# Performance work log

Hardware: AMD Instinct MI355X
Metric: run time of the kernel (lower is better)

The kernel has to match this reference:

```python
import jax, jax.numpy as jnp
import numpy as np

B, H, S, DK, DV = 4, 16, 8192, 128, 128

def setup_inputs() -> dict:
    key = jax.random.key(0)
    k1, k2, k3, k4 = jax.random.split(key, 4)
    return {
        "K": jax.random.normal(k1, (B, H, S, DK), dtype=jnp.float32),
        "V": jax.random.normal(k2, (B, H, S, DV), dtype=jnp.float32),
        "M": jax.random.normal(k3, (B, H, DK, DV), dtype=jnp.float32),
        "z": jax.random.uniform(k4, (B, H, DK), dtype=jnp.float32),
    }

def reference(K, V, M, z):
    # phi = ELU(K) + 1  (positive feature map)
    phi_K = jax.nn.elu(K) + 1.0                                   # (B,H,S,dk)
    V_existing = jnp.einsum('bhsk,bhkv->bhsv', phi_K, M)          # (B,H,S,dv)
    delta_M = jnp.einsum('bhsk,bhsv->bhkv', phi_K, V - V_existing)
    new_M = M + delta_M                                           # (B,H,dk,dv)
    new_z = z + phi_K.sum(axis=-2)                                # (B,H,dk)
    return new_M, new_z
```

## Files before the change

kernel.cpp:

```cpp
#include <hip/hip_runtime.h>

#define BH 64
#define SEQ 8192
#define DK 128
#define DV 128
#define CS 64
#define LR 72

typedef _Float16 f16;
typedef _Float16 f16x4 __attribute__((ext_vector_type(4)));
typedef _Float16 f16x8 __attribute__((ext_vector_type(8)));
typedef float f32x4 __attribute__((ext_vector_type(4)));

template <int NC, bool PARTIAL>
__global__ __launch_bounds__(512, 4) void delta_phase1(
    const float* __restrict__ Kg, const float* __restrict__ Vg,
    float* __restrict__ dstP,
    float* __restrict__ dstG,
    float* __restrict__ newZ)
{
  __shared__ f16 phi_lds[DK * LR];
  __shared__ f16 v_lds[DV * LR];

  constexpr int SC  = SEQ / NC;
  constexpr int NST = SC / CS;

  const int chunk = blockIdx.x;
  const int bh    = blockIdx.y;
  const int tid   = threadIdx.x;
  const int wave  = tid >> 6;
  const int lane  = tid & 63;
  const int l31   = lane & 31;
  const int lhi   = lane >> 5;
  const int f15_  = lane & 15;
  const int quad  = lane >> 4;

  const float* Kh = Kg + ((size_t)bh * SEQ + (size_t)chunk * SC) * DK;
  const float* Vh = Vg + ((size_t)bh * SEQ + (size_t)chunk * SC) * DV;
  const int srow = wave * 8 + lhi * 4;

  f32x4 acc[8][2];
#pragma unroll
  for (int r = 0; r < 8; ++r)
#pragma unroll
    for (int c = 0; c < 2; ++c)
      acc[r][c] = (f32x4){0.f, 0.f, 0.f, 0.f};

  float zacc[4] = {0.f, 0.f, 0.f, 0.f};

  float kr[16], vr[16];
#define LOAD_STAGE(ST)                                              \
  {                                                                 \
    const float* Ks_ = Kh + (size_t)(ST) * CS * DK;                 \
    const float* Vs_ = Vh + (size_t)(ST) * CS * DV;                 \
    _Pragma("unroll")                                               \
    for (int fj = 0; fj < 4; ++fj) {                                \
      const int feat_ = fj * 32 + l31;                              \
      const float* kp_ = Ks_ + (size_t)srow * DK + feat_;           \
      const float* vp_ = Vs_ + (size_t)srow * DV + feat_;           \
      _Pragma("unroll")                                             \
      for (int j = 0; j < 4; ++j) {                                 \
        kr[fj * 4 + j] = kp_[(size_t)j * DK];                       \
        vr[fj * 4 + j] = vp_[(size_t)j * DV];                       \
      }                                                             \
    }                                                               \
  }

  LOAD_STAGE(0);

  for (int st = 0; st < NST; ++st) {
#pragma unroll
    for (int fj = 0; fj < 4; ++fj) {
      const int feat = fj * 32 + l31;
      const float a0 = kr[fj * 4 + 0];
      const float a1 = kr[fj * 4 + 1];
      const float a2 = kr[fj * 4 + 2];
      const float a3 = kr[fj * 4 + 3];
      const float p0 = a0 > 0.f ? a0 + 1.f : __expf(a0);
      const float p1 = a1 > 0.f ? a1 + 1.f : __expf(a1);
      const float p2 = a2 > 0.f ? a2 + 1.f : __expf(a2);
      const float p3 = a3 > 0.f ? a3 + 1.f : __expf(a3);
      zacc[fj] += (p0 + p1) + (p2 + p3);
      *(f16x4*)&phi_lds[feat * LR + srow] =
          (f16x4){(f16)p0, (f16)p1, (f16)p2, (f16)p3};
      *(f16x4*)&v_lds[feat * LR + srow] =
          (f16x4){(f16)vr[fj * 4 + 0], (f16)vr[fj * 4 + 1],
                  (f16)vr[fj * 4 + 2], (f16)vr[fj * 4 + 3]};
    }
    __syncthreads();

    if (st + 1 < NST) LOAD_STAGE(st + 1);

    const f16* bsrc  = (wave < 4) ? v_lds : phi_lds;
    const int  cbase = (wave < 4) ? wave * 32 : wave * 32 - 128;
    __builtin_amdgcn_s_setprio(1);
#pragma unroll
    for (int ss = 0; ss < 2; ++ss) {
      const int sb = ss * 32 + quad * 8;
      f16x8 bfr[2];
#pragma unroll
      for (int c = 0; c < 2; ++c)
        bfr[c] = *(const f16x8*)&bsrc[(cbase + c * 16 + f15_) * LR + sb];
#pragma unroll
      for (int r = 0; r < 8; ++r) {
        const f16x8 afr = *(const f16x8*)&phi_lds[(r * 16 + f15_) * LR + sb];
        acc[r][0] = __builtin_amdgcn_mfma_f32_16x16x32_f16(afr, bfr[0], acc[r][0], 0, 0, 0);
        acc[r][1] = __builtin_amdgcn_mfma_f32_16x16x32_f16(afr, bfr[1], acc[r][1], 0, 0, 0);
      }
    }
    __builtin_amdgcn_s_setprio(0);
    __syncthreads();
  }
#undef LOAD_STAGE

  if (PARTIAL) {
    const size_t pb = (size_t)(bh * NC + chunk) * (128 * 256);
#pragma unroll
    for (int r = 0; r < 8; ++r)
#pragma unroll
      for (int c = 0; c < 2; ++c) {
        const int col = wave * 32 + c * 16 + f15_;
#pragma unroll
        for (int q = 0; q < 4; ++q) {
          const int row = r * 16 + quad * 4 + q;
          dstP[pb + (size_t)row * 256 + col] = acc[r][c][q];
        }
      }
  } else {
    const size_t mb = (size_t)bh * DK * DV;
#pragma unroll
    for (int r = 0; r < 8; ++r)
#pragma unroll
      for (int c = 0; c < 2; ++c) {
        const int col = wave * 32 + c * 16 + f15_;
#pragma unroll
        for (int q = 0; q < 4; ++q) {
          const int row = r * 16 + quad * 4 + q;
          const float v = acc[r][c][q];
          if (col < DV)
            atomicAdd(&dstP[mb + (size_t)row * DV + col], v);
          else
            atomicAdd(&dstG[mb + (size_t)row * DK + (col - DV)], v);
        }
      }
  }
#pragma unroll
  for (int fj = 0; fj < 4; ++fj) {
    float v = zacc[fj];
    v += __shfl_xor(v, 32, 64);
    if (lhi == 0) atomicAdd(&newZ[bh * DK + fj * 32 + l31], v);
  }
}

__global__ __launch_bounds__(256) void delta_reduce(
    const float* __restrict__ Pp, const float* __restrict__ Mg,
    float* __restrict__ newM, float* __restrict__ Gred, int NC)
{
  const int ct  = blockIdx.x;
  const int bh  = blockIdx.y;
  const int tid = threadIdx.x;
  const int col = ct * 32 + (tid & 31);
  const int r0  = tid >> 5;

  float acc[16];
#pragma unroll
  for (int i = 0; i < 16; ++i) acc[i] = 0.f;

  const float* base = Pp + (size_t)(bh * NC) * 32768;
  for (int ch = 0; ch < NC; ++ch) {
    const float* p = base + (size_t)ch * 32768;
#pragma unroll
    for (int i = 0; i < 16; ++i)
      acc[i] += p[(size_t)(r0 + 8 * i) * 256 + col];
  }
  if (col < 128) {
#pragma unroll
    for (int i = 0; i < 16; ++i) {
      const int row = r0 + 8 * i;
      newM[(size_t)bh * 16384 + (size_t)row * 128 + col] =
          Mg[(size_t)bh * 16384 + (size_t)row * 128 + col] + acc[i];
    }
  } else {
#pragma unroll
    for (int i = 0; i < 16; ++i) {
      const int row = r0 + 8 * i;
      Gred[(size_t)bh * 16384 + (size_t)row * 128 + (col - 128)] = acc[i];
    }
  }
}

__global__ __launch_bounds__(256) void delta_gm(
    const float* __restrict__ Mg, const float* __restrict__ G, float* __restrict__ newM)
{
  __shared__ float Gs[64 * 129];
  __shared__ float Ms[DK * 32];
  const int sub = blockIdx.x;
  const int bh  = blockIdx.y;
  const int kh  = sub >> 2;
  const int vt  = sub & 3;
  const int tid = threadIdx.x;
  const size_t mb = (size_t)bh * DK * DV;

  for (int i = tid; i < 64 * DK; i += 256)
    Gs[(i >> 7) * 129 + (i & 127)] = G[mb + (size_t)(kh * 64 + (i >> 7)) * DK + (i & 127)];
  for (int i = tid; i < DK * 32; i += 256)
    Ms[i] = Mg[mb + (size_t)(i >> 5) * DV + vt * 32 + (i & 31)];
  __syncthreads();

  const int kl = tid >> 2;
  const int vs = (tid & 3) * 8;
  float a[8];
#pragma unroll
  for (int j = 0; j < 8; ++j) a[j] = 0.f;
  for (int kk = 0; kk < DK; ++kk) {
    const float g = Gs[kl * 129 + kk];
#pragma unroll
    for (int j = 0; j < 8; ++j) a[j] += g * Ms[kk * 32 + vs + j];
  }
  float* dst = &newM[mb + (size_t)(kh * 64 + kl) * DV + vt * 32 + vs];
#pragma unroll
  for (int j = 0; j < 8; ++j) dst[j] -= a[j];
}

extern "C" void kernel_launch(void* const* d_in, const int* in_sizes, int n_in,
                              void* d_out, int out_size, void* d_ws, size_t ws_size,
                              hipStream_t stream) {
  const float* Kg = (const float*)d_in[0];
  const float* Vg = (const float*)d_in[1];
  const float* Mg = (const float*)d_in[2];
  const float* zg = (const float*)d_in[3];
  float* out  = (float*)d_out;
  float* newM = out;
  float* newZ = out + (size_t)BH * DK * DV;

  const size_t gredF = (size_t)BH * DK * DK;
  const size_t need8 = ((size_t)BH * 8 * 32768 + gredF) * sizeof(float);

  hipMemcpyAsync(newZ, zg, sizeof(float) * (size_t)BH * DK,
                 hipMemcpyDeviceToDevice, stream);

  if (ws_size >= need8) {
    float* Pp   = (float*)d_ws;
    float* Gred = Pp + (size_t)BH * 8 * 32768;
    delta_phase1<8, true><<<dim3(8, BH), 512, 0, stream>>>(Kg, Vg, Pp, nullptr, newZ);
    delta_reduce<<<dim3(8, BH), 256, 0, stream>>>(Pp, Mg, newM, Gred, 8);
    delta_gm<<<dim3(8, BH), 256, 0, stream>>>(Mg, Gred, newM);
  } else {
    float* Gws = (float*)d_ws;
    hipMemcpyAsync(newM, Mg, sizeof(float) * (size_t)BH * DK * DV,
                   hipMemcpyDeviceToDevice, stream);
    hipMemsetAsync(Gws, 0, sizeof(float) * gredF, stream);
    delta_phase1<8, false><<<dim3(8, BH), 512, 0, stream>>>(Kg, Vg, newM, Gws, newZ);
    delta_gm<<<dim3(8, BH), 256, 0, stream>>>(Mg, Gws, newM);
  }
}
```

Baseline: 565.6 us.

## Use float4 loads, smaller stages with register double-buffering, and XOR-swizzled LDS

Phase 1 now processes 32-row stages instead of 64. Each thread issues vectorized float4 global loads of four consecutive features, rather than strided scalar loads. Two register sets alternate so the next stage loads while the current one converts and runs MFMA, and barriers are raw s_barrier calls with lgkmcnt waits. LDS indices are XOR-swizzled to reduce bank conflicts on the transposed f16x2 stores and f16x8 reads. The cost is more barriers per row processed and less MFMA work per stage.

```diff
diff --git a/kernel.cpp b/kernel.cpp
--- a/kernel.cpp
+++ b/kernel.cpp
@@ -4,11 +4,11 @@
 #define SEQ 8192
 #define DK 128
 #define DV 128
-#define CS 64
+#define CS 32
 #define LR 72
 
 typedef _Float16 f16;
-typedef _Float16 f16x4 __attribute__((ext_vector_type(4)));
+typedef _Float16 f16x2 __attribute__((ext_vector_type(2)));
 typedef _Float16 f16x8 __attribute__((ext_vector_type(8)));
 typedef float f32x4 __attribute__((ext_vector_type(4)));
 
@@ -24,20 +24,24 @@
 
   constexpr int SC  = SEQ / NC;
   constexpr int NST = SC / CS;
+  static_assert(NST % 2 == 0, "double-buffer needs even stage count");
 
   const int chunk = blockIdx.x;
   const int bh    = blockIdx.y;
   const int tid   = threadIdx.x;
   const int wave  = tid >> 6;
   const int lane  = tid & 63;
-  const int l31   = lane & 31;
-  const int lhi   = lane >> 5;
+  const int c32   = lane & 31;
+  const int chi   = lane >> 5;
   const int f15_  = lane & 15;
   const int quad  = lane >> 4;
 
   const float* Kh = Kg + ((size_t)bh * SEQ + (size_t)chunk * SC) * DK;
   const float* Vh = Vg + ((size_t)bh * SEQ + (size_t)chunk * SC) * DV;
-  const int srow = wave * 8 + lhi * 4;
+
+  const int srow0    = wave * 4 + chi * 2;
+  const int featbase = c32 * 4;
+  const int swx      = ((c32 >> 1) & 7) << 3;
 
   f32x4 acc[8][2];
 #pragma unroll
@@ -48,70 +52,80 @@
 
   float zacc[4] = {0.f, 0.f, 0.f, 0.f};
 
-  float kr[16], vr[16];
-#define LOAD_STAGE(ST)                                              \
-  {                                                                 \
-    const float* Ks_ = Kh + (size_t)(ST) * CS * DK;                 \
-    const float* Vs_ = Vh + (size_t)(ST) * CS * DV;                 \
-    _Pragma("unroll")                                               \
-    for (int fj = 0; fj < 4; ++fj) {                                \
-      const int feat_ = fj * 32 + l31;                              \
-      const float* kp_ = Ks_ + (size_t)srow * DK + feat_;           \
-      const float* vp_ = Vs_ + (size_t)srow * DV + feat_;           \
-      _Pragma("unroll")                                             \
-      for (int j = 0; j < 4; ++j) {                                 \
-        kr[fj * 4 + j] = kp_[(size_t)j * DK];                       \
-        vr[fj * 4 + j] = vp_[(size_t)j * DV];                       \
-      }                                                             \
-    }                                                               \
-  }
-
-  LOAD_STAGE(0);
-
-  for (int st = 0; st < NST; ++st) {
-#pragma unroll
-    for (int fj = 0; fj < 4; ++fj) {
-      const int feat = fj * 32 + l31;
-      const float a0 = kr[fj * 4 + 0];
-      const float a1 = kr[fj * 4 + 1];
-      const float a2 = kr[fj * 4 + 2];
-      const float a3 = kr[fj * 4 + 3];
-      const float p0 = a0 > 0.f ? a0 + 1.f : __expf(a0);
-      const float p1 = a1 > 0.f ? a1 + 1.f : __expf(a1);
-      const float p2 = a2 > 0.f ? a2 + 1.f : __expf(a2);
-      const float p3 = a3 > 0.f ? a3 + 1.f : __expf(a3);
-      zacc[fj] += (p0 + p1) + (p2 + p3);
-      *(f16x4*)&phi_lds[feat * LR + srow] =
-          (f16x4){(f16)p0, (f16)p1, (f16)p2, (f16)p3};
-      *(f16x4*)&v_lds[feat * LR + srow] =
-          (f16x4){(f16)vr[fj * 4 + 0], (f16)vr[fj * 4 + 1],
-                  (f16)vr[fj * 4 + 2], (f16)vr[fj * 4 + 3]};
-    }
-    __syncthreads();
-
-    if (st + 1 < NST) LOAD_STAGE(st + 1);
-
-    const f16* bsrc  = (wave < 4) ? v_lds : phi_lds;
-    const int  cbase = (wave < 4) ? wave * 32 : wave * 32 - 128;
-    __builtin_amdgcn_s_setprio(1);
-#pragma unroll
-    for (int ss = 0; ss < 2; ++ss) {
-      const int sb = ss * 32 + quad * 8;
-      f16x8 bfr[2];
-#pragma unroll
-      for (int c = 0; c < 2; ++c)
-        bfr[c] = *(const f16x8*)&bsrc[(cbase + c * 16 + f15_) * LR + sb];
-#pragma unroll
-      for (int r = 0; r < 8; ++r) {
-        const f16x8 afr = *(const f16x8*)&phi_lds[(r * 16 + f15_) * LR + sb];
-        acc[r][0] = __builtin_amdgcn_mfma_f32_16x16x32_f16(afr, bfr[0], acc[r][0], 0, 0, 0);
-        acc[r][1] = __builtin_amdgcn_mfma_f32_16x16x32_f16(afr, bfr[1], acc[r][1], 0, 0, 0);
-      }
-    }
-    __builtin_amdgcn_s_setprio(0);
-    __syncthreads();
+  f32x4 ka0, ka1, va0, va1;
+  f32x4 kb0, kb1, vb0, vb1;
+
+#define LOAD_STAGE(ST, K0, K1, V0, V1)                                   \
+  {                                                                      \
+    const float* kp_ = Kh + ((size_t)(ST) * CS + srow0) * DK + featbase; \
+    const float* vp_ = Vh + ((size_t)(ST) * CS + srow0) * DV + featbase; \
+    K0 = *(const f32x4*)kp_;                                             \
+    K1 = *(const f32x4*)(kp_ + DK);                                      \
+    V0 = *(const f32x4*)vp_;                                             \
+    V1 = *(const f32x4*)(vp_ + DV);                                      \
+  }
+
+#define CONVERT_STORE(K0, K1, V0, V1)                                    \
+  {                                                                      \
+    _Pragma("unroll")                                                    \
+    for (int ff = 0; ff < 4; ++ff) {                                     \
+      const int feat = featbase + ff;                                    \
+      const float a0 = K0[ff], a1 = K1[ff];                              \
+      const float p0 = a0 > 0.f ? a0 + 1.f : __expf(a0);                 \
+      const float p1 = a1 > 0.f ? a1 + 1.f : __expf(a1);                 \
+      zacc[ff] += p0 + p1;                                               \
+      const int idx = (feat * LR + srow0) ^ swx;                         \
+      *(f16x2*)&phi_lds[idx] = (f16x2){(f16)p0, (f16)p1};                \
+      *(f16x2*)&v_lds[idx]   = (f16x2){(f16)V0[ff], (f16)V1[ff]};        \
+    }                                                                    \
+  }
+
+#define BAR()                                                            \
+  {                                                                      \
+    asm volatile("s_waitcnt lgkmcnt(0)" ::: "memory");                   \
+    __builtin_amdgcn_s_barrier();                                        \
+  }
+
+#define MFMA_PHASE()                                                     \
+  {                                                                      \
+    const f16* bsrc  = (wave < 4) ? v_lds : phi_lds;                     \
+    const int  cbase = (wave < 4) ? wave * 32 : wave * 32 - 128;         \
+    const int  sb    = quad * 8;                                         \
+    __builtin_amdgcn_s_setprio(1);                                       \
+    f16x8 bfr[2];                                                        \
+    _Pragma("unroll")                                                    \
+    for (int c = 0; c < 2; ++c) {                                        \
+      const int fB = cbase + c * 16 + f15_;                              \
+      bfr[c] = *(const f16x8*)&bsrc[(fB * LR + sb) ^ (((fB >> 3) & 7) << 3)]; \
+    }                                                                    \
+    _Pragma("unroll")                                                    \
+    for (int r = 0; r < 8; ++r) {                                        \
+      const int fA = r * 16 + f15_;                                      \
+      const f16x8 afr = *(const f16x8*)&phi_lds[(fA * LR + sb) ^ (((fA >> 3) & 7) << 3)]; \
+      acc[r][0] = __builtin_amdgcn_mfma_f32_16x16x32_f16(afr, bfr[0], acc[r][0], 0, 0, 0); \
+      acc[r][1] = __builtin_amdgcn_mfma_f32_16x16x32_f16(afr, bfr[1], acc[r][1], 0, 0, 0); \
+    }                                                                    \
+    __builtin_amdgcn_s_setprio(0);                                       \
+  }
+
+  LOAD_STAGE(0, ka0, ka1, va0, va1);
+
+  for (int st = 0; st < NST; st += 2) {
+    LOAD_STAGE(st + 1, kb0, kb1, vb0, vb1);
+    CONVERT_STORE(ka0, ka1, va0, va1);
+    BAR();
+    MFMA_PHASE();
+    BAR();
+    if (st + 2 < NST) LOAD_STAGE(st + 2, ka0, ka1, va0, va1);
+    CONVERT_STORE(kb0, kb1, vb0, vb1);
+    BAR();
+    MFMA_PHASE();
+    BAR();
   }
 #undef LOAD_STAGE
+#undef CONVERT_STORE
+#undef BAR
+#undef MFMA_PHASE
 
   if (PARTIAL) {
     const size_t pb = (size_t)(bh * NC + chunk) * (128 * 256);
@@ -145,10 +159,10 @@
       }
   }
 #pragma unroll
-  for (int fj = 0; fj < 4; ++fj) {
-    float v = zacc[fj];
+  for (int ff = 0; ff < 4; ++ff) {
+    float v = zacc[ff];
     v += __shfl_xor(v, 32, 64);
-    if (lhi == 0) atomicAdd(&newZ[bh * DK + fj * 32 + l31], v);
+    if (chi == 0) atomicAdd(&newZ[bh * DK + featbase + ff], v);
   }
 }
 
```

Measured after the change: 693.4 us. 22.6% more time.
